# Kernel tuning notes

Measured on AMD Instinct MI355X. Metric: run time of the kernel, lower is better.

Reference implementation:

```python
import jax, jax.numpy as jnp
import numpy as np

N_SRC = 32768
N_DST = 32768
E = 524288
SRC_D = 64
DST_D = 64
EDGE_D = 16
OUT_D = 128
HEADS = 8
IN_D = SRC_D + DST_D + EDGE_D  # 144


def _lin_init(k, i, o):
    return jax.random.normal(k, (i, o), jnp.float32) * (1.0 / np.sqrt(i))


def setup_inputs() -> dict:
    key = jax.random.key(0)
    ks = jax.random.split(key, 12)
    return {
        "x_src": jax.random.normal(ks[0], (N_SRC, SRC_D), jnp.float32),
        "x_dst": jax.random.normal(ks[1], (N_DST, DST_D), jnp.float32),
        "edge_attr": jax.random.normal(ks[2], (E, EDGE_D), jnp.float32),
        "edge_index": jax.random.randint(ks[3], (2, E), 0, N_DST, dtype=jnp.int64),
        "q": jax.random.uniform(ks[4], (1, OUT_D), jnp.float32) * 0.1,
        "k_w0": _lin_init(ks[5], IN_D, OUT_D), "k_b0": jnp.zeros((OUT_D,), jnp.float32),
        "k_w1": _lin_init(ks[6], OUT_D, OUT_D), "k_b1": jnp.zeros((OUT_D,), jnp.float32),
        "v_w0": _lin_init(ks[7], IN_D, OUT_D), "v_b0": jnp.zeros((OUT_D,), jnp.float32),
        "v_w1": _lin_init(ks[8], OUT_D, OUT_D), "v_b1": jnp.zeros((OUT_D,), jnp.float32),
        "o_w0": _lin_init(ks[9], OUT_D, OUT_D), "o_b0": jnp.zeros((OUT_D,), jnp.float32),
        "o_w1": _lin_init(ks[10], OUT_D, OUT_D), "o_b1": jnp.zeros((OUT_D,), jnp.float32),
    }


def _res_stack(x, w0, b0, w1, b1, last_activation):
    # ResidualStack(n_residuals=2): input linear + relu, then one residual linear block
    h = jax.nn.relu(x @ w0 + b0)
    h = h + (h @ w1 + b1)
    return jax.nn.relu(h) if last_activation else h


def reference(x_src, x_dst, edge_attr, edge_index, q,
              k_w0, k_b0, k_w1, k_b1,
              v_w0, v_b0, v_w1, v_b1,
              o_w0, o_b0, o_w1, o_b1):
    src, dst = edge_index[0], edge_index[1]
    # gather per-edge features: [E, IN_D]
    x = jnp.concatenate([x_src[src], x_dst[dst], edge_attr], axis=-1)
    k = _res_stack(x, k_w0, k_b0, k_w1, k_b1, False)   # [E, OUT_D]
    v = _res_stack(x, v_w0, v_b0, v_w1, v_b1, False)   # [E, OUT_D]
    d = OUT_D // HEADS
    qh = q.reshape(HEADS, d)
    kh = k.reshape(E, HEADS, d)
    scores = jnp.einsum('hd,ehd->eh', qh, kh) / jnp.sqrt(jnp.float32(d))  # [E, H]
    # segment softmax over destination-node neighborhoods
    seg_max = jax.ops.segment_max(scores, dst, num_segments=N_DST)
    seg_max = jnp.where(jnp.isfinite(seg_max), seg_max, jnp.float32(0.0))
    ex = jnp.exp(scores - seg_max[dst])
    denom = jax.ops.segment_sum(ex, dst, num_segments=N_DST)
    attn = ex / (denom[dst] + jnp.float32(1e-16))      # [E, H]
    msg = (attn[:, :, None] * v.reshape(E, HEADS, d)).reshape(E, OUT_D)
    aggr = jax.ops.segment_sum(msg, dst, num_segments=N_DST)  # [N_DST, OUT_D]
    out = _res_stack(jax.nn.relu(aggr), o_w0, o_b0, o_w1, o_b1, True)
    return out
```

## Files before the change

### kernel.cpp

```cpp
#include <hip/hip_runtime.h>
#include <math.h>

#define NSRC 32768
#define NDST 32768
#define NE 524288
#define SRC_D 64
#define DST_D 64
#define EDGE_D 16
#define IN_DIM 144
#define OUT_DIM 128
#define HEADS 8
#define HD 16

#define HS_LD 264

__global__ __launch_bounds__(128) void build_A_kernel(
    const float* __restrict__ q, const float* __restrict__ k_w1,
    const float* __restrict__ k_b1, float* __restrict__ A, float* __restrict__ C,
    float* __restrict__ At)
{
    const int j = threadIdx.x;
    #pragma unroll
    for (int h = 0; h < HEADS; ++h) {
        float s = 0.f;
        #pragma unroll
        for (int d = 0; d < HD; ++d)
            s = fmaf(k_w1[j*OUT_DIM + h*HD + d], q[h*HD + d], s);
        if ((j >> 4) == h) s += q[j];
        const float a = 0.25f * s;
        A[j*HEADS + h] = a;
        At[h*OUT_DIM + j] = a;
    }
    if (j < HEADS) {
        float s = 0.f;
        #pragma unroll
        for (int d = 0; d < HD; ++d) s = fmaf(q[j*HD + d], k_b1[j*HD + d], s);
        C[j] = 0.25f * s;
    }
}

__global__ __launch_bounds__(256) void edge_kernel(
    const float* __restrict__ x_src, const float* __restrict__ x_dst,
    const float* __restrict__ e_attr, const int* __restrict__ eidx,
    const float* __restrict__ k_w0, const float* __restrict__ k_b0,
    const float* __restrict__ v_w0, const float* __restrict__ v_b0,
    const float* __restrict__ v_w1, const float* __restrict__ v_b1,
    const float* __restrict__ At, const float* __restrict__ C,
    float* __restrict__ acc_g, float* __restrict__ denom_g)
{
    __shared__ float xs[32][IN_DIM];
    __shared__ float Hs[32][HS_LD];
    __shared__ float exs[32][HEADS];
    __shared__ int   dsts[32];

    const int t = threadIdx.x;
    const int e0 = blockIdx.x * 32;

    {
        const int g = t >> 3, l8 = t & 7;
        const int e = e0 + g;
        const int si = eidx[e];
        const int di = eidx[NE + e];
        if (l8 == 0) dsts[g] = di;
        const float4* ps = (const float4*)(x_src + (size_t)si * SRC_D);
        float4 a0 = ps[l8*2+0], a1 = ps[l8*2+1];
        *(float4*)&xs[g][l8*8+0] = a0;
        *(float4*)&xs[g][l8*8+4] = a1;
        const float4* pd = (const float4*)(x_dst + (size_t)di * DST_D);
        float4 b0 = pd[l8*2+0], b1 = pd[l8*2+1];
        *(float4*)&xs[g][SRC_D + l8*8+0] = b0;
        *(float4*)&xs[g][SRC_D + l8*8+4] = b1;
        const float2* pe = (const float2*)(e_attr + (size_t)e * EDGE_D);
        float2 c0v = pe[l8];
        *(float2*)&xs[g][SRC_D + DST_D + l8*2] = c0v;
    }
    __syncthreads();

    {
        const int cq = t & 63;
        const int c0 = cq * 4;
        const int g  = t >> 6;
        const bool isK = (c0 < OUT_DIM);
        const float4* __restrict__ Wf4 =
            (const float4*)(isK ? k_w0 : v_w0) + ((isK ? c0 : c0 - OUT_DIM) >> 2);
        const float4 bias = *((const float4*)(isK ? k_b0 : v_b0) + ((isK ? c0 : c0 - OUT_DIM) >> 2));

        float4 acc[8];
        #pragma unroll
        for (int e = 0; e < 8; ++e) acc[e] = make_float4(0.f, 0.f, 0.f, 0.f);

        #pragma unroll 4
        for (int i = 0; i < IN_DIM; i += 4) {
            const float4 wa = Wf4[(i+0) * (OUT_DIM/4)];
            const float4 wb = Wf4[(i+1) * (OUT_DIM/4)];
            const float4 wc = Wf4[(i+2) * (OUT_DIM/4)];
            const float4 wd = Wf4[(i+3) * (OUT_DIM/4)];
            #pragma unroll
            for (int e = 0; e < 8; ++e) {
                const float4 xv = *(const float4*)&xs[g*8 + e][i];
                acc[e].x = fmaf(xv.x, wa.x, acc[e].x);
                acc[e].y = fmaf(xv.x, wa.y, acc[e].y);
                acc[e].z = fmaf(xv.x, wa.z, acc[e].z);
                acc[e].w = fmaf(xv.x, wa.w, acc[e].w);
                acc[e].x = fmaf(xv.y, wb.x, acc[e].x);
                acc[e].y = fmaf(xv.y, wb.y, acc[e].y);
                acc[e].z = fmaf(xv.y, wb.z, acc[e].z);
                acc[e].w = fmaf(xv.y, wb.w, acc[e].w);
                acc[e].x = fmaf(xv.z, wc.x, acc[e].x);
                acc[e].y = fmaf(xv.z, wc.y, acc[e].y);
                acc[e].z = fmaf(xv.z, wc.z, acc[e].z);
                acc[e].w = fmaf(xv.z, wc.w, acc[e].w);
                acc[e].x = fmaf(xv.w, wd.x, acc[e].x);
                acc[e].y = fmaf(xv.w, wd.y, acc[e].y);
                acc[e].z = fmaf(xv.w, wd.z, acc[e].z);
                acc[e].w = fmaf(xv.w, wd.w, acc[e].w);
            }
        }
        #pragma unroll
        for (int e = 0; e < 8; ++e) {
            float4 h;
            h.x = fmaxf(acc[e].x + bias.x, 0.f);
            h.y = fmaxf(acc[e].y + bias.y, 0.f);
            h.z = fmaxf(acc[e].z + bias.z, 0.f);
            h.w = fmaxf(acc[e].w + bias.w, 0.f);
            *(float4*)&Hs[g*8 + e][c0] = h;
        }
    }
    __syncthreads();

    const int cq2 = t & 31;
    const int c0v = cq2 * 4;
    const int g2  = t >> 5;
    float4 vacc[4];
    {
        const float4* __restrict__ Vf4 = (const float4*)v_w1 + cq2;
        #pragma unroll
        for (int e = 0; e < 4; ++e) vacc[e] = make_float4(0.f, 0.f, 0.f, 0.f);
        #pragma unroll 4
        for (int j = 0; j < OUT_DIM; j += 4) {
            const float4 wa = Vf4[(j+0) * (OUT_DIM/4)];
            const float4 wb = Vf4[(j+1) * (OUT_DIM/4)];
            const float4 wc = Vf4[(j+2) * (OUT_DIM/4)];
            const float4 wd = Vf4[(j+3) * (OUT_DIM/4)];
            #pragma unroll
            for (int e = 0; e < 4; ++e) {
                const float4 hv = *(const float4*)&Hs[g2*4 + e][OUT_DIM + j];
                vacc[e].x = fmaf(hv.x, wa.x, vacc[e].x);
                vacc[e].y = fmaf(hv.x, wa.y, vacc[e].y);
                vacc[e].z = fmaf(hv.x, wa.z, vacc[e].z);
                vacc[e].w = fmaf(hv.x, wa.w, vacc[e].w);
                vacc[e].x = fmaf(hv.y, wb.x, vacc[e].x);
                vacc[e].y = fmaf(hv.y, wb.y, vacc[e].y);
                vacc[e].z = fmaf(hv.y, wb.z, vacc[e].z);
                vacc[e].w = fmaf(hv.y, wb.w, vacc[e].w);
                vacc[e].x = fmaf(hv.z, wc.x, vacc[e].x);
                vacc[e].y = fmaf(hv.z, wc.y, vacc[e].y);
                vacc[e].z = fmaf(hv.z, wc.z, vacc[e].z);
                vacc[e].w = fmaf(hv.z, wc.w, vacc[e].w);
                vacc[e].x = fmaf(hv.w, wd.x, vacc[e].x);
                vacc[e].y = fmaf(hv.w, wd.y, vacc[e].y);
                vacc[e].z = fmaf(hv.w, wd.z, vacc[e].z);
                vacc[e].w = fmaf(hv.w, wd.w, vacc[e].w);
            }
        }
    }

    {
        const int se = t >> 3;
        const int sh = t & 7;
        const float4* __restrict__ At4 = (const float4*)(At + sh * OUT_DIM);
        float s = C[sh];
        #pragma unroll 4
        for (int j = 0; j < OUT_DIM; j += 4) {
            const float4 hk = *(const float4*)&Hs[se][j];
            const float4 av = At4[j >> 2];
            s = fmaf(hk.x, av.x, s);
            s = fmaf(hk.y, av.y, s);
            s = fmaf(hk.z, av.z, s);
            s = fmaf(hk.w, av.w, s);
        }
        const float ex = __expf(s);
        exs[se][sh] = ex;
        atomicAdd(&denom_g[(size_t)dsts[se]*HEADS + sh], ex);
    }
    __syncthreads();

    {
        const float4 bv = *((const float4*)v_b1 + cq2);
        const int h = c0v >> 4;
        #pragma unroll
        for (int e = 0; e < 4; ++e) {
            const int ee = g2*4 + e;
            const float4 hv = *(const float4*)&Hs[ee][OUT_DIM + c0v];
            const float ex = exs[ee][h];
            const size_t base = (size_t)dsts[ee]*OUT_DIM + c0v;
            atomicAdd(&acc_g[base+0], ex * (hv.x + vacc[e].x + bv.x));
            atomicAdd(&acc_g[base+1], ex * (hv.y + vacc[e].y + bv.y));
            atomicAdd(&acc_g[base+2], ex * (hv.z + vacc[e].z + bv.z));
            atomicAdd(&acc_g[base+3], ex * (hv.w + vacc[e].w + bv.w));
        }
    }
}

__global__ __launch_bounds__(256) void node_kernel(
    const float* __restrict__ acc_g, const float* __restrict__ denom_g,
    const float* __restrict__ o_w0, const float* __restrict__ o_b0,
    const float* __restrict__ o_w1, const float* __restrict__ o_b1,
    float* __restrict__ out)
{
    __shared__ float as[32][OUT_DIM];
    __shared__ float hs[32][OUT_DIM];
    const int t = threadIdx.x;
    const int n0 = blockIdx.x * 32;

    for (int r = t; r < 32*32; r += 256) {
        const int n = r >> 5, c4 = r & 31;
        float4 a = *(const float4*)&acc_g[(size_t)(n0+n)*OUT_DIM + c4*4];
        const float d = denom_g[(size_t)(n0+n)*HEADS + (c4 >> 2)] + 1e-16f;
        a.x = fmaxf(a.x / d, 0.f);
        a.y = fmaxf(a.y / d, 0.f);
        a.z = fmaxf(a.z / d, 0.f);
        a.w = fmaxf(a.w / d, 0.f);
        *(float4*)&as[n][c4*4] = a;
    }
    __syncthreads();

    const int cc = t & (OUT_DIM-1);
    const int half = t >> 7;
    float hreg[16];
    {
        float acc1[16];
        #pragma unroll
        for (int e2 = 0; e2 < 16; ++e2) acc1[e2] = 0.f;
        for (int j = 0; j < OUT_DIM; j += 4) {
            const float w0v = o_w0[(j+0)*OUT_DIM + cc];
            const float w1v = o_w0[(j+1)*OUT_DIM + cc];
            const float w2v = o_w0[(j+2)*OUT_DIM + cc];
            const float w3v = o_w0[(j+3)*OUT_DIM + cc];
            #pragma unroll
            for (int e2 = 0; e2 < 16; ++e2) {
                const float4 av = *(const float4*)&as[half*16 + e2][j];
                acc1[e2] = fmaf(av.x, w0v, acc1[e2]);
                acc1[e2] = fmaf(av.y, w1v, acc1[e2]);
                acc1[e2] = fmaf(av.z, w2v, acc1[e2]);
                acc1[e2] = fmaf(av.w, w3v, acc1[e2]);
            }
        }
        const float bv = o_b0[cc];
        #pragma unroll
        for (int e2 = 0; e2 < 16; ++e2) {
            float h = fmaxf(acc1[e2] + bv, 0.f);
            hreg[e2] = h;
            hs[half*16 + e2][cc] = h;
        }
    }
    __syncthreads();
    {
        float acc2[16];
        #pragma unroll
        for (int e2 = 0; e2 < 16; ++e2) acc2[e2] = 0.f;
        for (int j = 0; j < OUT_DIM; j += 4) {
            const float w0v = o_w1[(j+0)*OUT_DIM + cc];
            const float w1v = o_w1[(j+1)*OUT_DIM + cc];
            const float w2v = o_w1[(j+2)*OUT_DIM + cc];
            const float w3v = o_w1[(j+3)*OUT_DIM + cc];
            #pragma unroll
            for (int e2 = 0; e2 < 16; ++e2) {
                const float4 hv = *(const float4*)&hs[half*16 + e2][j];
                acc2[e2] = fmaf(hv.x, w0v, acc2[e2]);
                acc2[e2] = fmaf(hv.y, w1v, acc2[e2]);
                acc2[e2] = fmaf(hv.z, w2v, acc2[e2]);
                acc2[e2] = fmaf(hv.w, w3v, acc2[e2]);
            }
        }
        const float bv = o_b1[cc];
        #pragma unroll
        for (int e2 = 0; e2 < 16; ++e2) {
            const int n = n0 + half*16 + e2;
            out[(size_t)n*OUT_DIM + cc] = fmaxf(hreg[e2] + acc2[e2] + bv, 0.f);
        }
    }
}

extern "C" void kernel_launch(void* const* d_in, const int* in_sizes, int n_in,
                              void* d_out, int out_size, void* d_ws, size_t ws_size,
                              hipStream_t stream) {
    const float* x_src  = (const float*)d_in[0];
    const float* x_dst  = (const float*)d_in[1];
    const float* e_attr = (const float*)d_in[2];
    const int*   eidx   = (const int*)  d_in[3];
    const float* q      = (const float*)d_in[4];
    const float* k_w0   = (const float*)d_in[5];
    const float* k_b0   = (const float*)d_in[6];
    const float* k_w1   = (const float*)d_in[7];
    const float* k_b1   = (const float*)d_in[8];
    const float* v_w0   = (const float*)d_in[9];
    const float* v_b0   = (const float*)d_in[10];
    const float* v_w1   = (const float*)d_in[11];
    const float* v_b1   = (const float*)d_in[12];
    const float* o_w0   = (const float*)d_in[13];
    const float* o_b0   = (const float*)d_in[14];
    const float* o_w1   = (const float*)d_in[15];
    const float* o_b1   = (const float*)d_in[16];
    float* out = (float*)d_out;

    float* acc_g   = (float*)d_ws;
    float* denom_g = acc_g + (size_t)NDST*OUT_DIM;
    float* A       = denom_g + (size_t)NDST*HEADS;
    float* C       = A + 128*HEADS;
    float* At      = C + 8;

    hipMemsetAsync(d_ws, 0, ((size_t)NDST*OUT_DIM + (size_t)NDST*HEADS)*sizeof(float), stream);

    build_A_kernel<<<1, 128, 0, stream>>>(q, k_w1, k_b1, A, C, At);
    edge_kernel<<<NE/32, 256, 0, stream>>>(x_src, x_dst, e_attr, eidx,
                                           k_w0, k_b0, v_w0, v_b0, v_w1, v_b1,
                                           At, C, acc_g, denom_g);
    node_kernel<<<NDST/32, 256, 0, stream>>>(acc_g, denom_g,
                                             o_w0, o_b0, o_w1, o_b1, out);
}
```

Before: 1.224 ms.

## Use split-bf16 MFMA for the first edge-layer GEMM with prepacked weights

Replaces the scalar-FMA first linear layer (144→256, K and V together) in the edge kernel with bf16 MFMA 16x16x32 instructions. Each input is split into a hi and a lo bf16 part, and three MFMA products are summed to approximate fp32 accuracy. A new prepack kernel converts the k_w0/v_w0 weights into the MFMA fragment layout ahead of time. Edge features are stored in LDS as hi/lo bf16 with K padded to 160. This trades scalar FMA throughput for matrix-core throughput, at the cost of extra conversion work, three MFMAs per product and a small loss of precision. The diff also adds an occupancy hint to launch_bounds and drops the unused A buffer.

```diff
diff --git a/kernel.cpp b/kernel.cpp
--- a/kernel.cpp
+++ b/kernel.cpp
@@ -13,11 +13,38 @@
 #define HD 16
 
 #define HS_LD 264
+#define K_PAD 168
+#define NKS 5
+
+typedef __attribute__((ext_vector_type(8))) short short8;
+typedef __attribute__((ext_vector_type(4))) float f32x4;
+
+__device__ __forceinline__ ushort bf_hi(float x) {
+    uint u = __float_as_uint(x);
+    return (ushort)((u + 0x7FFF + ((u >> 16) & 1)) >> 16);
+}
+__device__ __forceinline__ float bf_f(ushort h) { return __uint_as_float(((uint)h) << 16); }
+
+__device__ __forceinline__ void pack8(const float* v, uint4* phi, uint4* plo) {
+    ushort h[8], l[8];
+    #pragma unroll
+    for (int j = 0; j < 8; ++j) {
+        h[j] = bf_hi(v[j]);
+        l[j] = bf_hi(v[j] - bf_f(h[j]));
+    }
+    phi->x = (uint)h[0] | ((uint)h[1] << 16);
+    phi->y = (uint)h[2] | ((uint)h[3] << 16);
+    phi->z = (uint)h[4] | ((uint)h[5] << 16);
+    phi->w = (uint)h[6] | ((uint)h[7] << 16);
+    plo->x = (uint)l[0] | ((uint)l[1] << 16);
+    plo->y = (uint)l[2] | ((uint)l[3] << 16);
+    plo->z = (uint)l[4] | ((uint)l[5] << 16);
+    plo->w = (uint)l[6] | ((uint)l[7] << 16);
+}
 
 __global__ __launch_bounds__(128) void build_A_kernel(
     const float* __restrict__ q, const float* __restrict__ k_w1,
-    const float* __restrict__ k_b1, float* __restrict__ A, float* __restrict__ C,
-    float* __restrict__ At)
+    const float* __restrict__ k_b1, float* __restrict__ C, float* __restrict__ At)
 {
     const int j = threadIdx.x;
     #pragma unroll
@@ -27,9 +54,7 @@
         for (int d = 0; d < HD; ++d)
             s = fmaf(k_w1[j*OUT_DIM + h*HD + d], q[h*HD + d], s);
         if ((j >> 4) == h) s += q[j];
-        const float a = 0.25f * s;
-        A[j*HEADS + h] = a;
-        At[h*OUT_DIM + j] = a;
+        At[h*OUT_DIM + j] = 0.25f * s;
     }
     if (j < HEADS) {
         float s = 0.f;
@@ -39,16 +64,42 @@
     }
 }
 
-__global__ __launch_bounds__(256) void edge_kernel(
+__global__ __launch_bounds__(256) void prepack_B_kernel(
+    const float* __restrict__ k_w0, const float* __restrict__ v_w0,
+    uint4* __restrict__ bhi, uint4* __restrict__ blo)
+{
+    const int tid = blockIdx.x * 256 + threadIdx.x;
+    const int fg = tid >> 6;
+    if (fg >= 16 * NKS) return;
+    const int lane = tid & 63;
+    const int ntg = fg / NKS, ks = fg % NKS;
+    const int ch = ntg * 16 + (lane & 15);
+    const int kb = ks * 32 + (lane >> 4) * 8;
+    float v[8];
+    #pragma unroll
+    for (int j = 0; j < 8; ++j) {
+        const int k = kb + j;
+        v[j] = (k < IN_DIM) ? (ch < OUT_DIM ? k_w0[k*OUT_DIM + ch]
+                                            : v_w0[k*OUT_DIM + ch - OUT_DIM])
+                            : 0.f;
+    }
+    uint4 h4, l4;
+    pack8(v, &h4, &l4);
+    bhi[fg*64 + lane] = h4;
+    blo[fg*64 + lane] = l4;
+}
+
+__global__ __launch_bounds__(256, 2) void edge_kernel(
     const float* __restrict__ x_src, const float* __restrict__ x_dst,
     const float* __restrict__ e_attr, const int* __restrict__ eidx,
-    const float* __restrict__ k_w0, const float* __restrict__ k_b0,
-    const float* __restrict__ v_w0, const float* __restrict__ v_b0,
+    const float* __restrict__ k_b0, const float* __restrict__ v_b0,
     const float* __restrict__ v_w1, const float* __restrict__ v_b1,
+    const uint4* __restrict__ Bph, const uint4* __restrict__ Bpl,
     const float* __restrict__ At, const float* __restrict__ C,
     float* __restrict__ acc_g, float* __restrict__ denom_g)
 {
-    __shared__ float xs[32][IN_DIM];
+    __shared__ ushort Ah[32][K_PAD];
+    __shared__ ushort Al[32][K_PAD];
     __shared__ float Hs[32][HS_LD];
     __shared__ float exs[32][HEADS];
     __shared__ int   dsts[32];
@@ -62,68 +113,83 @@
         const int si = eidx[e];
         const int di = eidx[NE + e];
         if (l8 == 0) dsts[g] = di;
-        const float4* ps = (const float4*)(x_src + (size_t)si * SRC_D);
-        float4 a0 = ps[l8*2+0], a1 = ps[l8*2+1];
-        *(float4*)&xs[g][l8*8+0] = a0;
-        *(float4*)&xs[g][l8*8+4] = a1;
-        const float4* pd = (const float4*)(x_dst + (size_t)di * DST_D);
-        float4 b0 = pd[l8*2+0], b1 = pd[l8*2+1];
-        *(float4*)&xs[g][SRC_D + l8*8+0] = b0;
-        *(float4*)&xs[g][SRC_D + l8*8+4] = b1;
-        const float2* pe = (const float2*)(e_attr + (size_t)e * EDGE_D);
-        float2 c0v = pe[l8];
-        *(float2*)&xs[g][SRC_D + DST_D + l8*2] = c0v;
-    }
-    __syncthreads();
-
-    {
-        const int cq = t & 63;
-        const int c0 = cq * 4;
-        const int g  = t >> 6;
-        const bool isK = (c0 < OUT_DIM);
-        const float4* __restrict__ Wf4 =
-            (const float4*)(isK ? k_w0 : v_w0) + ((isK ? c0 : c0 - OUT_DIM) >> 2);
-        const float4 bias = *((const float4*)(isK ? k_b0 : v_b0) + ((isK ? c0 : c0 - OUT_DIM) >> 2));
-
-        float4 acc[8];
-        #pragma unroll
-        for (int e = 0; e < 8; ++e) acc[e] = make_float4(0.f, 0.f, 0.f, 0.f);
-
-        #pragma unroll 4
-        for (int i = 0; i < IN_DIM; i += 4) {
-            const float4 wa = Wf4[(i+0) * (OUT_DIM/4)];
-            const float4 wb = Wf4[(i+1) * (OUT_DIM/4)];
-            const float4 wc = Wf4[(i+2) * (OUT_DIM/4)];
-            const float4 wd = Wf4[(i+3) * (OUT_DIM/4)];
-            #pragma unroll
-            for (int e = 0; e < 8; ++e) {
-                const float4 xv = *(const float4*)&xs[g*8 + e][i];
-                acc[e].x = fmaf(xv.x, wa.x, acc[e].x);
-                acc[e].y = fmaf(xv.x, wa.y, acc[e].y);
-                acc[e].z = fmaf(xv.x, wa.z, acc[e].z);
-                acc[e].w = fmaf(xv.x, wa.w, acc[e].w);
-                acc[e].x = fmaf(xv.y, wb.x, acc[e].x);
-                acc[e].y = fmaf(xv.y, wb.y, acc[e].y);
-                acc[e].z = fmaf(xv.y, wb.z, acc[e].z);
-                acc[e].w = fmaf(xv.y, wb.w, acc[e].w);
-                acc[e].x = fmaf(xv.z, wc.x, acc[e].x);
-                acc[e].y = fmaf(xv.z, wc.y, acc[e].y);
-                acc[e].z = fmaf(xv.z, wc.z, acc[e].z);
-                acc[e].w = fmaf(xv.z, wc.w, acc[e].w);
-                acc[e].x = fmaf(xv.w, wd.x, acc[e].x);
-                acc[e].y = fmaf(xv.w, wd.y, acc[e].y);
-                acc[e].z = fmaf(xv.w, wd.z, acc[e].z);
-                acc[e].w = fmaf(xv.w, wd.w, acc[e].w);
-            }
-        }
-        #pragma unroll
-        for (int e = 0; e < 8; ++e) {
-            float4 h;
-            h.x = fmaxf(acc[e].x + bias.x, 0.f);
-            h.y = fmaxf(acc[e].y + bias.y, 0.f);
-            h.z = fmaxf(acc[e].z + bias.z, 0.f);
-            h.w = fmaxf(acc[e].w + bias.w, 0.f);
-            *(float4*)&Hs[g*8 + e][c0] = h;
+        float v8[8];
+        uint4 h4, l4;
+        {
+            const float4* ps = (const float4*)(x_src + (size_t)si * SRC_D);
+            float4 a0 = ps[l8*2+0], a1 = ps[l8*2+1];
+            v8[0]=a0.x; v8[1]=a0.y; v8[2]=a0.z; v8[3]=a0.w;
+            v8[4]=a1.x; v8[5]=a1.y; v8[6]=a1.z; v8[7]=a1.w;
+            pack8(v8, &h4, &l4);
+            *(uint4*)&Ah[g][l8*8] = h4;
+            *(uint4*)&Al[g][l8*8] = l4;
+        }
+        {
+            const float4* pd = (const float4*)(x_dst + (size_t)di * DST_D);
+            float4 b0 = pd[l8*2+0], b1 = pd[l8*2+1];
+            v8[0]=b0.x; v8[1]=b0.y; v8[2]=b0.z; v8[3]=b0.w;
+            v8[4]=b1.x; v8[5]=b1.y; v8[6]=b1.z; v8[7]=b1.w;
+            pack8(v8, &h4, &l4);
+            *(uint4*)&Ah[g][SRC_D + l8*8] = h4;
+            *(uint4*)&Al[g][SRC_D + l8*8] = l4;
+        }
+        {
+            const float2* pe = (const float2*)(e_attr + (size_t)e * EDGE_D);
+            float2 c2 = pe[l8];
+            ushort h0 = bf_hi(c2.x), h1 = bf_hi(c2.y);
+            ushort l0 = bf_hi(c2.x - bf_f(h0)), l1 = bf_hi(c2.y - bf_f(h1));
+            *(uint*)&Ah[g][SRC_D + DST_D + l8*2] = (uint)h0 | ((uint)h1 << 16);
+            *(uint*)&Al[g][SRC_D + DST_D + l8*2] = (uint)l0 | ((uint)l1 << 16);
+        }
+        if (l8 < 2) {
+            const uint4 z = make_uint4(0u, 0u, 0u, 0u);
+            *(uint4*)&Ah[g][IN_DIM + l8*8] = z;
+            *(uint4*)&Al[g][IN_DIM + l8*8] = z;
+        }
+    }
+    __syncthreads();
+
+    {
+        const int w = t >> 6, l = t & 63;
+        const int r16 = l & 15, kq = l >> 4;
+        f32x4 acc[4][2];
+        #pragma unroll
+        for (int nt = 0; nt < 4; ++nt) {
+            acc[nt][0] = (f32x4){0.f, 0.f, 0.f, 0.f};
+            acc[nt][1] = (f32x4){0.f, 0.f, 0.f, 0.f};
+        }
+        #pragma unroll
+        for (int ks = 0; ks < NKS; ++ks) {
+            const int koff = ks*32 + kq*8;
+            const short8 ah0 = *(const short8*)&Ah[r16][koff];
+            const short8 al0 = *(const short8*)&Al[r16][koff];
+            const short8 ah1 = *(const short8*)&Ah[16 + r16][koff];
+            const short8 al1 = *(const short8*)&Al[16 + r16][koff];
+            #pragma unroll
+            for (int nt = 0; nt < 4; ++nt) {
+                const int fg = ((w*4 + nt)*NKS + ks)*64 + l;
+                const short8 bh = *(const short8*)&Bph[fg];
+                const short8 bl = *(const short8*)&Bpl[fg];
+                acc[nt][0] = __builtin_amdgcn_mfma_f32_16x16x32_bf16(al0, bh, acc[nt][0], 0, 0, 0);
+                acc[nt][0] = __builtin_amdgcn_mfma_f32_16x16x32_bf16(ah0, bl, acc[nt][0], 0, 0, 0);
+                acc[nt][0] = __builtin_amdgcn_mfma_f32_16x16x32_bf16(ah0, bh, acc[nt][0], 0, 0, 0);
+                acc[nt][1] = __builtin_amdgcn_mfma_f32_16x16x32_bf16(al1, bh, acc[nt][1], 0, 0, 0);
+                acc[nt][1] = __builtin_amdgcn_mfma_f32_16x16x32_bf16(ah1, bl, acc[nt][1], 0, 0, 0);
+                acc[nt][1] = __builtin_amdgcn_mfma_f32_16x16x32_bf16(ah1, bh, acc[nt][1], 0, 0, 0);
+            }
+        }
+        #pragma unroll
+        for (int nt = 0; nt < 4; ++nt) {
+            const int ch = (w*4 + nt)*16 + r16;
+            const float bias = (ch < OUT_DIM) ? k_b0[ch] : v_b0[ch - OUT_DIM];
+            #pragma unroll
+            for (int mt = 0; mt < 2; ++mt) {
+                #pragma unroll
+                for (int r = 0; r < 4; ++r) {
+                    const int edge = mt*16 + kq*4 + r;
+                    Hs[edge][ch] = fmaxf(acc[nt][mt][r] + bias, 0.f);
+                }
+            }
         }
     }
     __syncthreads();
@@ -306,16 +372,19 @@
 
     float* acc_g   = (float*)d_ws;
     float* denom_g = acc_g + (size_t)NDST*OUT_DIM;
-    float* A       = denom_g + (size_t)NDST*HEADS;
-    float* C       = A + 128*HEADS;
+    float* C       = denom_g + (size_t)NDST*HEADS;
     float* At      = C + 8;
+    size_t boff = ((size_t)NDST*OUT_DIM + (size_t)NDST*HEADS + 8 + 8*OUT_DIM + 3) & ~(size_t)3;
+    uint4* Bph = (uint4*)((float*)d_ws + boff);
+    uint4* Bpl = Bph + 16*NKS*64;
 
     hipMemsetAsync(d_ws, 0, ((size_t)NDST*OUT_DIM + (size_t)NDST*HEADS)*sizeof(float), stream);
 
-    build_A_kernel<<<1, 128, 0, stream>>>(q, k_w1, k_b1, A, C, At);
+    build_A_kernel<<<1, 128, 0, stream>>>(q, k_w1, k_b1, C, At);
+    prepack_B_kernel<<<20, 256, 0, stream>>>(k_w0, v_w0, Bph, Bpl);
     edge_kernel<<<NE/32, 256, 0, stream>>>(x_src, x_dst, e_attr, eidx,
-                                           k_w0, k_b0, v_w0, v_b0, v_w1, v_b1,
-                                           At, C, acc_g, denom_g);
+                                           k_b0, v_b0, v_w1, v_b1,
+                                           Bph, Bpl, At, C, acc_g, denom_g);
     node_kernel<<<NDST/32, 256, 0, stream>>>(acc_g, denom_g,
                                              o_w0, o_b0, o_w1, o_b1, out);
 }
```

Result: faster. 1.166 ms (-4.8%).
